# Optimization experiments

Measured on AMD Instinct MI355X. Metric: run time of the kernel, lower is better.

Reference implementation:

```python
import jax, jax.numpy as jnp
import numpy as np

B, N, F, H, HEADS = 2, 256, 64, 64, 4
C = HEADS * H  # n_coefficients (coefficients_mlp is Identity => must equal n_heads*hidden)
EPS = 1e-5
INF = 1e5


def _lin(key, fan_in, fan_out, bias=True):
    k1, k2 = jax.random.split(key)
    w = jax.random.normal(k1, (fan_in, fan_out), jnp.float32) * (1.0 / np.sqrt(fan_in))
    if bias:
        b = jax.random.normal(k2, (fan_out,), jnp.float32) * 0.01
        return w, b
    return w


def setup_inputs() -> dict:
    key = jax.random.key(0)
    ks = jax.random.split(key, 16)
    inp = dict(
        h=jax.random.normal(ks[0], (B, N, F), jnp.float32),
        x=jax.random.normal(ks[1], (B, N, 3), jnp.float32),
        v=jax.random.normal(ks[2], (B, N, 3), jnp.float32),
    )
    inp['edge_w1'], inp['edge_b1'] = _lin(ks[3], 2 * F + 1, H)
    inp['edge_w2'], inp['edge_b2'] = _lin(ks[4], H, H)
    inp['sem_w'], inp['sem_b'] = _lin(ks[5], H, HEADS)
    inp['post_w1'], inp['post_b1'] = _lin(ks[6], C, H)
    inp['post_w2'], inp['post_b2'] = _lin(ks[7], H, H)
    inp['node_w1'], inp['node_b1'] = _lin(ks[8], C + H + F, H)
    inp['node_w2'], inp['node_b2'] = _lin(ks[9], H, F)
    inp['vel_w1'], inp['vel_b1'] = _lin(ks[10], F, H)
    inp['vel_w2'] = _lin(ks[11], H, 1, bias=False) * 0.001  # xavier gain=0.001 analogue
    inp['vmix_w'] = _lin(ks[12], C, 1, bias=False)[:, 0]
    inp['log_gamma'] = -jnp.log(jnp.linspace(1.0, 5.0, HEADS)).astype(jnp.float32)
    return inp


def reference(h, x, v, edge_w1, edge_b1, edge_w2, edge_b2, sem_w, sem_b,
              post_w1, post_b1, post_w2, post_b2, node_w1, node_b1,
              node_w2, node_b2, vel_w1, vel_b1, vel_w2, vmix_w, log_gamma):
    silu = jax.nn.silu
    n = h.shape[-2]
    eye = jnp.eye(n, dtype=h.dtype)[:, :, None]  # [N,N,1] diagonal mask

    # pairwise geometry: entry [i,j] = x_j - x_i
    x_minus_xt = x[..., None, :, :] - x[..., :, None, :]                # [B,N,N,3]
    x_norm = jnp.sqrt((x_minus_xt ** 2).sum(-1, keepdims=True) + EPS)   # [B,N,N,1]

    # pairwise node-feature concat (h_j, h_i) + distance -> edge MLP
    h_j = jnp.broadcast_to(h[..., None, :, :], (B, n, n, F))
    h_i = jnp.broadcast_to(h[..., :, None, :], (B, n, n, F))
    h_cat = jnp.concatenate([h_j, h_i, x_norm], axis=-1)                # [B,N,N,2F+1]
    h_e_mtx = silu(silu(h_cat @ edge_w1 + edge_b1) @ edge_w2 + edge_b2)  # [B,N,N,H]

    # euclidean attention: softmin over j of gamma*dist, diagonal masked out
    dist = (x_norm + INF * eye) * jnp.exp(log_gamma)                    # [B,N,N,heads]
    euclid_att = jax.nn.softmax(-dist, axis=-2)
    # semantic attention: LeakyReLU(0.2) logits, diagonal masked, softmax over j
    sem = jax.nn.leaky_relu(h_e_mtx @ sem_w + sem_b, 0.2) - INF * eye
    sem_att = jax.nn.softmax(sem, axis=-2)
    comb_att = jax.nn.softmax(euclid_att * sem_att, axis=-2)            # [B,N,N,heads]

    # attention-weighted edge features, flattened over (H, heads)
    h_e_att = (h_e_mtx[..., :, None] * comb_att[..., None, :]).reshape(B, n, n, C)

    # spatial attention (coefficients_mlp is Identity)
    unit = x_minus_xt / (x_norm + EPS)                                  # [B,N,N,3]
    # combinations.mean(dim=-3) without materializing [B,N,N,C,3]
    comb_sum = jnp.einsum('bijc,bijd->bicd', h_e_att, unit) / n         # [B,N,C,3]
    comb_norm = (comb_sum ** 2).sum(-1)                                 # [B,N,C]
    h_comb = silu(silu(comb_norm @ post_w1 + post_b1) @ post_w2 + post_b2)

    # delta_v = mean_j (v_mixing over C of combinations)
    delta_v = jnp.einsum('bijc,c,bijd->bid', h_e_att, vmix_w, unit) / n  # [B,N,3]

    h_agg = h_e_att.sum(axis=-2)                                        # sum over j -> [B,N,C]
    out = jnp.concatenate([h, h_agg, h_comb], axis=-1)
    out = silu(silu(out @ node_w1 + node_b1) @ node_w2 + node_b2)
    h_new = h + out                                                     # residual

    # coordinate / velocity update
    v_scale = silu(h_new @ vel_w1 + vel_b1) @ vel_w2                    # [B,N,1]
    v_new = delta_v + v_scale * v
    x_new = x + v_new
    return h_new, x_new, v_new
```

## Files before the change

### kernel.cpp

```cpp
#include <hip/hip_runtime.h>
#include <hip/hip_bf16.h>
#include <math.h>

#define EPSV 1e-5f
#define INFV 1e5f

typedef short bf16x8 __attribute__((ext_vector_type(8)));
typedef float f32x4 __attribute__((ext_vector_type(4)));

__device__ __forceinline__ float rcp_f(float x) { return __builtin_amdgcn_rcpf(x); }
__device__ __forceinline__ float silu_f(float v) { return v * rcp_f(1.0f + __expf(-v)); }

__device__ __forceinline__ unsigned short f2bf(float f) {
  unsigned int u = __float_as_uint(f);
  u = (u + 0x7fffu + ((u >> 16) & 1u)) >> 16;
  return (unsigned short)u;
}
__device__ __forceinline__ float bf2f(unsigned short h) {
  return __uint_as_float(((unsigned int)h) << 16);
}
__device__ __forceinline__ unsigned int pkbf(float a, float b) {
  float2 f2; f2.x = a; f2.y = b;
  __hip_bfloat162 t = __float22bfloat162_rn(f2);
  unsigned int u;
  __builtin_memcpy(&u, &t, 4);
  return u;
}

__device__ __forceinline__ void gemm64(const unsigned short* A_lds, const unsigned short* B_lds,
                                       int w, int l15, int quad, f32x4 acc[4][4]) {
#pragma unroll
  for (int tr = 0; tr < 4; ++tr)
#pragma unroll
    for (int tc = 0; tc < 4; ++tc)
      acc[tr][tc] = (f32x4){0.f, 0.f, 0.f, 0.f};
#pragma unroll
  for (int ms = 0; ms < 64; ms += 32) {
    bf16x8 af[4], bfr[4];
#pragma unroll
    for (int tr = 0; tr < 4; ++tr)
      af[tr] = *reinterpret_cast<const bf16x8*>(&A_lds[(64 * w + 16 * tr + l15) * 72 + ms + quad * 8]);
#pragma unroll
    for (int tc = 0; tc < 4; ++tc)
      bfr[tc] = *reinterpret_cast<const bf16x8*>(&B_lds[(16 * tc + l15) * 72 + ms + quad * 8]);
#pragma unroll
    for (int tr = 0; tr < 4; ++tr)
#pragma unroll
      for (int tc = 0; tc < 4; ++tc)
        acc[tr][tc] = __builtin_amdgcn_mfma_f32_16x16x32_bf16(af[tr], bfr[tc], acc[tr][tc], 0, 0, 0);
  }
}

__global__ __launch_bounds__(512, 2) void k_all(
    const float* __restrict__ h, const float* __restrict__ x, const float* __restrict__ v,
    const float* __restrict__ ew1, const float* __restrict__ eb1,
    const float* __restrict__ ew2, const float* __restrict__ eb2,
    const float* __restrict__ semw, const float* __restrict__ semb,
    const float* __restrict__ pw1, const float* __restrict__ pb1,
    const float* __restrict__ pw2, const float* __restrict__ pb2,
    const float* __restrict__ nw1, const float* __restrict__ nb1,
    const float* __restrict__ nw2, const float* __restrict__ nb2,
    const float* __restrict__ vw1, const float* __restrict__ vb1,
    const float* __restrict__ vw2, const float* __restrict__ vmix,
    const float* __restrict__ lgam, float* __restrict__ out) {

  __shared__ __align__(16) unsigned short TH0[256 * 72];
  __shared__ __align__(16) unsigned short TH1[256 * 72];
  __shared__ __align__(16) char R0[9216];
  __shared__ __align__(16) char R1[9216];
  __shared__ __align__(16) float SD1[2048];
  __shared__ __align__(16) unsigned short E3T[16 * 72];
  __shared__ __align__(16) float4 unit_l[2][256];
  __shared__ float w1dk[64];
  __shared__ float eb1l[64];
  __shared__ __align__(16) float bms[512];

  const int bid = blockIdx.x;
  const int b   = bid >> 7;
  const int ip  = bid & 127;
  const int tid = threadIdx.x;
  const int g   = tid >> 8;
  const int jt  = tid & 255;
  const int i_g = 2 * ip + g;
  const int bi  = (b << 8) | i_g;
  const int bj  = (b << 8) | jt;

  const int w8   = tid >> 6;
  const int lid  = tid & 63;
  const int wg   = w8 & 3;
  const int l15  = lid & 15;
  const int quad = lid >> 4;

  unsigned short* E2Ta = (unsigned short*)R0;
  unsigned short* E2Tb = (unsigned short*)R1;
  unsigned short* THg  = g ? TH1 : TH0;
  char* Rg = g ? R1 : R0;
  float*  sd_g  = g ? SD1 : (float*)R0;
  float4* cat_g = (float4*)Rg;
  float*  cn_g  = (float*)(Rg + 4096);
  float*  hag_g = (float*)(Rg + 5120);
  float4* scS   = (float4*)bms + g * 8;
  float4* scP   = (float4*)bms + 16 + g * 4;
  float4* scD   = (float4*)bms + 24 + g * 4;
  float*  dvs_g = bms + 128 + g * 4;

  const float xi0 = x[bi * 3 + 0], xi1 = x[bi * 3 + 1], xi2 = x[bi * 3 + 2];
  const float dx = x[bj * 3 + 0] - xi0;
  const float dy = x[bj * 3 + 1] - xi1;
  const float dz = x[bj * 3 + 2] - xi2;
  const float dn = sqrtf(dx * dx + dy * dy + dz * dz + EPSV);
  const float invn = rcp_f(dn + EPSV);
  const float ux = dx * invn, uy = dy * invn, uz = dz * invn;
  unit_l[g][jt] = make_float4(ux, uy, uz, dn);

  {
    const float4* hb4 = reinterpret_cast<const float4*>(h + (size_t)(b << 8) * 64);
#pragma unroll
    for (int q = 0; q < 8; ++q) {
      int idx = q * 512 + tid;
      float4 f4 = hb4[idx];
      int row = idx >> 4, c4 = idx & 15;
      uint2 pk;
      pk.x = pkbf(f4.x, f4.y);
      pk.y = pkbf(f4.z, f4.w);
      *reinterpret_cast<uint2*>(&TH0[row * 72 + c4 * 4]) = pk;
    }
  }
#pragma unroll
  for (int q = 0; q < 8; ++q) {
    int idx = q * 512 + tid;
    E2Ta[(idx & 63) * 72 + (idx >> 6)] = f2bf(ew1[idx]);
  }
#pragma unroll
  for (int q = 0; q < 8; ++q) {
    int idx = q * 512 + tid;
    E2Tb[(idx & 63) * 72 + (idx >> 6)] = f2bf(ew2[idx]);
  }
  {
    int n = tid >> 6, kk = tid & 63;
    E3T[n * 72 + kk] = f2bf((n < 4) ? semw[kk * 4 + n] : vmix[kk * 4 + (n - 4)]);
    E3T[(8 + n) * 72 + kk] = 0;
  }
  if (tid < 64) { w1dk[tid] = ew1[128 * 64 + tid]; eb1l[tid] = eb1[tid]; }
  {
    int s = jt >> 6, k = jt & 63;
    const float* hrow = h + (size_t)bi * 64;
    float bp = 0.f;
#pragma unroll
    for (int f2 = 0; f2 < 16; ++f2) {
      int f = s * 16 + f2;
      bp += hrow[f] * ew1[(64 + f) * 64 + k];
    }
    bms[g * 256 + s * 64 + k] = bp;
  }
  __syncthreads();

  f32x4 acc1[2][4];
#pragma unroll
  for (int tr = 0; tr < 2; ++tr)
#pragma unroll
    for (int tc = 0; tc < 4; ++tc)
      acc1[tr][tc] = (f32x4){0.f, 0.f, 0.f, 0.f};
#pragma unroll
  for (int ms = 0; ms < 64; ms += 32) {
    bf16x8 af[2], bfr[4];
#pragma unroll
    for (int tr = 0; tr < 2; ++tr)
      af[tr] = *reinterpret_cast<const bf16x8*>(&TH0[(32 * w8 + 16 * tr + l15) * 72 + ms + quad * 8]);
#pragma unroll
    for (int tc = 0; tc < 4; ++tc)
      bfr[tc] = *reinterpret_cast<const bf16x8*>(&E2Ta[(16 * tc + l15) * 72 + ms + quad * 8]);
#pragma unroll
    for (int tr = 0; tr < 2; ++tr)
#pragma unroll
      for (int tc = 0; tc < 4; ++tc)
        acc1[tr][tc] = __builtin_amdgcn_mfma_f32_16x16x32_bf16(af[tr], bfr[tc], acc1[tr][tc], 0, 0, 0);
  }

#pragma unroll
  for (int tc = 0; tc < 4; ++tc) {
    int kc = 16 * tc + l15;
    float wd = w1dk[kc];
    float eb = eb1l[kc];
    float ak0 = eb + bms[kc] + bms[64 + kc] + bms[128 + kc] + bms[192 + kc];
    float ak1 = eb + bms[256 + kc] + bms[320 + kc] + bms[384 + kc] + bms[448 + kc];
#pragma unroll
    for (int tr = 0; tr < 2; ++tr)
#pragma unroll
      for (int r = 0; r < 4; ++r) {
        int row = 32 * w8 + 16 * tr + quad * 4 + r;
        float a = acc1[tr][tc][r];
        float d0 = unit_l[0][row].w, d1 = unit_l[1][row].w;
        TH0[row * 72 + kc] = f2bf(silu_f(a + ak0 + d0 * wd));
        TH1[row * 72 + kc] = f2bf(silu_f(a + ak1 + d1 * wd));
      }
  }
  __syncthreads();

  f32x4 acc2[4][4];
  gemm64(THg, E2Tb, wg, l15, quad, acc2);
#pragma unroll
  for (int tc = 0; tc < 4; ++tc) {
    float b2 = eb2[16 * tc + l15];
#pragma unroll
    for (int tr = 0; tr < 4; ++tr)
#pragma unroll
      for (int r = 0; r < 4; ++r) {
        int row = 64 * wg + 16 * tr + quad * 4 + r;
        THg[row * 72 + 16 * tc + l15] = f2bf(silu_f(acc2[tr][tc][r] + b2));
      }
  }

  f32x4 acc3[4];
#pragma unroll
  for (int tr = 0; tr < 4; ++tr) acc3[tr] = (f32x4){0.f, 0.f, 0.f, 0.f};
#pragma unroll
  for (int ms = 0; ms < 64; ms += 32) {
    bf16x8 b3 = *reinterpret_cast<const bf16x8*>(&E3T[l15 * 72 + ms + quad * 8]);
#pragma unroll
    for (int tr = 0; tr < 4; ++tr) {
      bf16x8 a3 = *reinterpret_cast<const bf16x8*>(&THg[(64 * wg + 16 * tr + l15) * 72 + ms + quad * 8]);
      acc3[tr] = __builtin_amdgcn_mfma_f32_16x16x32_bf16(a3, b3, acc3[tr], 0, 0, 0);
    }
  }
  if (l15 < 8) {
#pragma unroll
    for (int tr = 0; tr < 4; ++tr)
#pragma unroll
      for (int r = 0; r < 4; ++r)
        sd_g[(64 * wg + 16 * tr + quad * 4 + r) * 8 + l15] = acc3[tr][r];
  }

  float4 s01 = *reinterpret_cast<const float4*>(sd_g + jt * 8);
  float4 s23 = *reinterpret_cast<const float4*>(sd_g + jt * 8 + 4);
  float4 sbv = *reinterpret_cast<const float4*>(semb);
  const float diag = (jt == i_g) ? INFV : 0.0f;
  float4 sl;
  sl.x = s01.x + sbv.x; sl.y = s01.y + sbv.y; sl.z = s01.z + sbv.z; sl.w = s01.w + sbv.w;
  sl.x = ((sl.x > 0.f) ? sl.x : 0.2f * sl.x) - diag;
  sl.y = ((sl.y > 0.f) ? sl.y : 0.2f * sl.y) - diag;
  sl.z = ((sl.z > 0.f) ? sl.z : 0.2f * sl.z) - diag;
  sl.w = ((sl.w > 0.f) ? sl.w : 0.2f * sl.w) - diag;

  float4 lg4 = *reinterpret_cast<const float4*>(lgam);
  const float dni = dn + diag;
  float4 e_eu = make_float4(__expf(-dni * __expf(lg4.x)), __expf(-dni * __expf(lg4.y)),
                            __expf(-dni * __expf(lg4.z)), __expf(-dni * __expf(lg4.w)));
  float4 e_sem = make_float4(__expf(sl.x), __expf(sl.y), __expf(sl.z), __expf(sl.w));

  float4 a8 = e_eu, b8 = e_sem;
#pragma unroll
  for (int off = 32; off >= 1; off >>= 1) {
    a8.x += __shfl_xor(a8.x, off); a8.y += __shfl_xor(a8.y, off);
    a8.z += __shfl_xor(a8.z, off); a8.w += __shfl_xor(a8.w, off);
    b8.x += __shfl_xor(b8.x, off); b8.y += __shfl_xor(b8.y, off);
    b8.z += __shfl_xor(b8.z, off); b8.w += __shfl_xor(b8.w, off);
  }
  if (lid == 0) { scS[wg] = a8; scS[4 + wg] = b8; }
  __syncthreads();
  float4 Se, Ss;
  {
    float4 r0 = scS[0], r1 = scS[1], r2 = scS[2], r3 = scS[3];
    Se = make_float4(r0.x + r1.x + r2.x + r3.x, r0.y + r1.y + r2.y + r3.y,
                     r0.z + r1.z + r2.z + r3.z, r0.w + r1.w + r2.w + r3.w);
    float4 s0 = scS[4], s1 = scS[5], s2 = scS[6], s3 = scS[7];
    Ss = make_float4(s0.x + s1.x + s2.x + s3.x, s0.y + s1.y + s2.y + s3.y,
                     s0.z + s1.z + s2.z + s3.z, s0.w + s1.w + s2.w + s3.w);
  }

  float4 p = make_float4((e_eu.x * rcp_f(Se.x)) * (e_sem.x * rcp_f(Ss.x)),
                         (e_eu.y * rcp_f(Se.y)) * (e_sem.y * rcp_f(Ss.y)),
                         (e_eu.z * rcp_f(Se.z)) * (e_sem.z * rcp_f(Ss.z)),
                         (e_eu.w * rcp_f(Se.w)) * (e_sem.w * rcp_f(Ss.w)));
  float4 ep = make_float4(__expf(p.x), __expf(p.y), __expf(p.z), __expf(p.w));
  float4 sp8 = ep;
#pragma unroll
  for (int off = 32; off >= 1; off >>= 1) {
    sp8.x += __shfl_xor(sp8.x, off); sp8.y += __shfl_xor(sp8.y, off);
    sp8.z += __shfl_xor(sp8.z, off); sp8.w += __shfl_xor(sp8.w, off);
  }
  if (lid == 0) scP[wg] = sp8;
  __syncthreads();
  float4 Sp;
  {
    float4 r0 = scP[0], r1 = scP[1], r2 = scP[2], r3 = scP[3];
    Sp = make_float4(r0.x + r1.x + r2.x + r3.x, r0.y + r1.y + r2.y + r3.y,
                     r0.z + r1.z + r2.z + r3.z, r0.w + r1.w + r2.w + r3.w);
  }
  float4 catt = make_float4(ep.x * rcp_f(Sp.x), ep.y * rcp_f(Sp.y),
                            ep.z * rcp_f(Sp.z), ep.w * rcp_f(Sp.w));
  cat_g[jt] = catt;

  float s = catt.x * s23.x + catt.y * s23.y + catt.z * s23.z + catt.w * s23.w;
  float dvx = s * ux, dvy = s * uy, dvz = s * uz;
#pragma unroll
  for (int off = 32; off >= 1; off >>= 1) {
    dvx += __shfl_xor(dvx, off); dvy += __shfl_xor(dvy, off); dvz += __shfl_xor(dvz, off);
  }
  if (lid == 0) scD[wg] = make_float4(dvx, dvy, dvz, 0.f);
  __syncthreads();
  if (jt == 0) {
    float4 r0 = scD[0], r1 = scD[1], r2 = scD[2], r3 = scD[3];
    const float inv = 1.0f / 256.0f;
    dvs_g[0] = (r0.x + r1.x + r2.x + r3.x) * inv;
    dvs_g[1] = (r0.y + r1.y + r2.y + r3.y) * inv;
    dvs_g[2] = (r0.z + r1.z + r2.z + r3.z) * inv;
  }

  {
    const int jg   = lid >> 2;
    const int ksub = lid & 3;
    const int kb   = 16 * wg + 4 * ksub;
    float agg[4][4], ax[4][4], ay[4][4], az[4][4];
#pragma unroll
    for (int kk = 0; kk < 4; ++kk)
#pragma unroll
      for (int hd = 0; hd < 4; ++hd) {
        agg[kk][hd] = 0.f; ax[kk][hd] = 0.f; ay[kk][hd] = 0.f; az[kk][hd] = 0.f;
      }
#pragma unroll 4
    for (int jr = 0; jr < 16; ++jr) {
      int jj = jr * 16 + jg;
      ushort4 hv4 = *reinterpret_cast<const ushort4*>(&THg[jj * 72 + kb]);
      float4 ca = cat_g[jj];
      float4 u  = unit_l[g][jj];
      float hev[4] = { bf2f(hv4.x), bf2f(hv4.y), bf2f(hv4.z), bf2f(hv4.w) };
#pragma unroll
      for (int kk = 0; kk < 4; ++kk) {
        float c0 = hev[kk] * ca.x, c1 = hev[kk] * ca.y, c2 = hev[kk] * ca.z, c3 = hev[kk] * ca.w;
        agg[kk][0] += c0; agg[kk][1] += c1; agg[kk][2] += c2; agg[kk][3] += c3;
        ax[kk][0] += c0 * u.x; ay[kk][0] += c0 * u.y; az[kk][0] += c0 * u.z;
        ax[kk][1] += c1 * u.x; ay[kk][1] += c1 * u.y; az[kk][1] += c1 * u.z;
        ax[kk][2] += c2 * u.x; ay[kk][2] += c2 * u.y; az[kk][2] += c2 * u.z;
        ax[kk][3] += c3 * u.x; ay[kk][3] += c3 * u.y; az[kk][3] += c3 * u.z;
      }
    }
#pragma unroll
    for (int off = 4; off <= 32; off <<= 1)
#pragma unroll
      for (int kk = 0; kk < 4; ++kk)
#pragma unroll
        for (int hd = 0; hd < 4; ++hd) {
          agg[kk][hd] += __shfl_xor(agg[kk][hd], off);
          ax[kk][hd]  += __shfl_xor(ax[kk][hd], off);
          ay[kk][hd]  += __shfl_xor(ay[kk][hd], off);
          az[kk][hd]  += __shfl_xor(az[kk][hd], off);
        }
    if (jg == 0) {
      const float inv = 1.0f / 256.0f;
#pragma unroll
      for (int kk = 0; kk < 4; ++kk) {
        int k = kb + kk;
        f32x4 cnv, hgv;
#pragma unroll
        for (int hd = 0; hd < 4; ++hd) {
          float cx = ax[kk][hd] * inv, cy = ay[kk][hd] * inv, cz = az[kk][hd] * inv;
          cnv[hd] = cx * cx + cy * cy + cz * cz;
          hgv[hd] = agg[kk][hd];
        }
        *reinterpret_cast<f32x4*>(&cn_g[k * 4])  = cnv;
        *reinterpret_cast<f32x4*>(&hag_g[k * 4]) = hgv;
      }
    }
  }
  __syncthreads();

  {
    const int k = lid;
    float* tmpg = (float*)THg;
    float a1 = 0.f;
#pragma unroll 16
    for (int m2 = 0; m2 < 64; ++m2) {
      int m = 64 * wg + m2;
      a1 += cn_g[m] * pw1[m * 64 + k];
    }
    tmpg[wg * 64 + k] = a1;
    if (wg == 1 || wg == 2) {
      float a2 = 0.f;
      int base = (wg - 1) * 128;
#pragma unroll 16
      for (int m2 = 0; m2 < 128; ++m2) {
        int m = base + m2;
        a2 += hag_g[m] * nw1[(64 + m) * 64 + k];
      }
      tmpg[256 + (wg - 1) * 64 + k] = a2;
    } else if (wg == 3) {
      float a2 = 0.f;
      const float* hrow = h + (size_t)bi * 64;
#pragma unroll 16
      for (int m = 0; m < 64; ++m) a2 += hrow[m] * nw1[m * 64 + k];
      tmpg[384 + k] = a2;
    }
  }
  __syncthreads();

  if (wg == 0) {
    const int k = lid;
    float* tmpg = (float*)THg;
    float* sh2  = tmpg + 512;

    float m1 = silu_f(pb1[k] + tmpg[k] + tmpg[64 + k] + tmpg[128 + k] + tmpg[192 + k]);
    sh2[k] = m1;

    float a = 0.f;
#pragma unroll 16
    for (int m = 0; m < 64; ++m) a += sh2[m] * pw2[m * 64 + k];
    float hcomb = silu_f(pb2[k] + a);
    sh2[64 + k] = hcomb;

    a = nb1[k] + tmpg[256 + k] + tmpg[320 + k] + tmpg[384 + k];
#pragma unroll 16
    for (int m = 0; m < 64; ++m) a += sh2[64 + m] * nw1[(320 + m) * 64 + k];
    sh2[128 + k] = silu_f(a);

    a = 0.f;
#pragma unroll 16
    for (int m = 0; m < 64; ++m) a += sh2[128 + m] * nw2[m * 64 + k];
    float hn = h[(size_t)bi * 64 + k] + silu_f(nb2[k] + a);
    out[(size_t)bi * 64 + k] = hn;
    sh2[192 + k] = hn;

    a = 0.f;
#pragma unroll 16
    for (int m = 0; m < 64; ++m) a += sh2[192 + m] * vw1[m * 64 + k];
    float vh = silu_f(vb1[k] + a) * vw2[k];
#pragma unroll
    for (int off = 32; off >= 1; off >>= 1) vh += __shfl_xor(vh, off);

    if (k == 0) {
      const float xi[3] = {xi0, xi1, xi2};
#pragma unroll
      for (int d = 0; d < 3; ++d) {
        float vn = dvs_g[d] + vh * v[bi * 3 + d];
        out[32768 + bi * 3 + d] = xi[d] + vn;
        out[34304 + bi * 3 + d] = vn;
      }
    }
  }
}

extern "C" void kernel_launch(void* const* d_in, const int* in_sizes, int n_in,
                              void* d_out, int out_size, void* d_ws, size_t ws_size,
                              hipStream_t stream) {
  const float* h    = (const float*)d_in[0];
  const float* x    = (const float*)d_in[1];
  const float* v    = (const float*)d_in[2];
  const float* ew1  = (const float*)d_in[3];
  const float* eb1  = (const float*)d_in[4];
  const float* ew2  = (const float*)d_in[5];
  const float* eb2  = (const float*)d_in[6];
  const float* semw = (const float*)d_in[7];
  const float* semb = (const float*)d_in[8];
  const float* pw1  = (const float*)d_in[9];
  const float* pb1  = (const float*)d_in[10];
  const float* pw2  = (const float*)d_in[11];
  const float* pb2  = (const float*)d_in[12];
  const float* nw1  = (const float*)d_in[13];
  const float* nb1  = (const float*)d_in[14];
  const float* nw2  = (const float*)d_in[15];
  const float* nb2  = (const float*)d_in[16];
  const float* vw1  = (const float*)d_in[17];
  const float* vb1  = (const float*)d_in[18];
  const float* vw2  = (const float*)d_in[19];
  const float* vmix = (const float*)d_in[20];
  const float* lgam = (const float*)d_in[21];
  float* out = (float*)d_out;

  k_all<<<256, 512, 0, stream>>>(h, x, v, ew1, eb1, ew2, eb2, semw, semb,
                                 pw1, pb1, pw2, pb2, nw1, nb1, nw2, nb2,
                                 vw1, vb1, vw2, vmix, lgam, out);
}
```

Measured before the change: 127.1 us.

## Process one node row per block with 256 threads and prefetch tail weights

Each block now handles a single row i with 256 threads, launching 512 blocks instead of 256 blocks of 512 threads that each covered two rows. The first edge-MLP layer goes back to the shared gemm64 helper, and the second LDS activation buffer and the split bias buffer are removed, which shrinks per-block shared memory and should let more blocks sit on each CU. The trade-off is that every block now reloads and converts the full h tile and the edge weight matrices for one row instead of two, doubling that setup work overall. The change also adds early warm-up loads of the node and post MLP weights, kept alive through an asm barrier, to pull them into cache before the serial tail.

```diff
diff --git a/kernel.cpp b/kernel.cpp
--- a/kernel.cpp
+++ b/kernel.cpp
@@ -51,7 +51,7 @@
   }
 }
 
-__global__ __launch_bounds__(512, 2) void k_all(
+__global__ __launch_bounds__(256, 2) void k_all(
     const float* __restrict__ h, const float* __restrict__ x, const float* __restrict__ v,
     const float* __restrict__ ew1, const float* __restrict__ eb1,
     const float* __restrict__ ew2, const float* __restrict__ eb2,
@@ -64,45 +64,49 @@
     const float* __restrict__ vw2, const float* __restrict__ vmix,
     const float* __restrict__ lgam, float* __restrict__ out) {
 
-  __shared__ __align__(16) unsigned short TH0[256 * 72];
-  __shared__ __align__(16) unsigned short TH1[256 * 72];
+  __shared__ __align__(16) unsigned short TH[256 * 72];
   __shared__ __align__(16) char R0[9216];
   __shared__ __align__(16) char R1[9216];
-  __shared__ __align__(16) float SD1[2048];
   __shared__ __align__(16) unsigned short E3T[16 * 72];
-  __shared__ __align__(16) float4 unit_l[2][256];
+  __shared__ __align__(16) float4 unit_l[256];
   __shared__ float w1dk[64];
   __shared__ float eb1l[64];
-  __shared__ __align__(16) float bms[512];
+  __shared__ __align__(16) float bms[256];
 
   const int bid = blockIdx.x;
-  const int b   = bid >> 7;
-  const int ip  = bid & 127;
+  const int b   = bid >> 8;
+  const int i   = bid & 255;
+  const int bi  = bid;
   const int tid = threadIdx.x;
-  const int g   = tid >> 8;
-  const int jt  = tid & 255;
-  const int i_g = 2 * ip + g;
-  const int bi  = (b << 8) | i_g;
-  const int bj  = (b << 8) | jt;
-
-  const int w8   = tid >> 6;
+  const int j   = tid;
+  const int bj  = (b << 8) | j;
+
+  const int w    = tid >> 6;
   const int lid  = tid & 63;
-  const int wg   = w8 & 3;
   const int l15  = lid & 15;
   const int quad = lid >> 4;
 
   unsigned short* E2Ta = (unsigned short*)R0;
   unsigned short* E2Tb = (unsigned short*)R1;
-  unsigned short* THg  = g ? TH1 : TH0;
-  char* Rg = g ? R1 : R0;
-  float*  sd_g  = g ? SD1 : (float*)R0;
-  float4* cat_g = (float4*)Rg;
-  float*  cn_g  = (float*)(Rg + 4096);
-  float*  hag_g = (float*)(Rg + 5120);
-  float4* scS   = (float4*)bms + g * 8;
-  float4* scP   = (float4*)bms + 16 + g * 4;
-  float4* scD   = (float4*)bms + 24 + g * 4;
-  float*  dvs_g = bms + 128 + g * 4;
+  float*  sd    = (float*)R0;
+  float4* cat_l = (float4*)R1;
+  float*  cn_l  = (float*)(R1 + 4096);
+  float*  hag_l = (float*)(R1 + 5120);
+  float4* scS   = (float4*)bms;
+  float4* scP   = (float4*)bms + 8;
+  float4* scD   = (float4*)bms + 12;
+  float*  dvs   = bms + 64;
+
+  float warm = 0.f;
+  {
+#pragma unroll
+    for (int q = 0; q < 4; ++q) warm += pw1[(4 * tid + q) * 16];
+#pragma unroll
+    for (int q = 0; q < 6; ++q) warm += nw1[(6 * tid + q) * 16];
+    warm += pw2[tid * 16] + nw2[tid * 16] + vw1[tid * 16];
+    if (tid < 64) warm += eb2[tid] + pb1[tid] + pb2[tid] + nb1[tid] +
+                          nb2[tid] + vb1[tid] + vw2[tid];
+  }
 
   const float xi0 = x[bi * 3 + 0], xi1 = x[bi * 3 + 1], xi2 = x[bi * 3 + 2];
   const float dx = x[bj * 3 + 0] - xi0;
@@ -111,39 +115,41 @@
   const float dn = sqrtf(dx * dx + dy * dy + dz * dz + EPSV);
   const float invn = rcp_f(dn + EPSV);
   const float ux = dx * invn, uy = dy * invn, uz = dz * invn;
-  unit_l[g][jt] = make_float4(ux, uy, uz, dn);
+  unit_l[j] = make_float4(ux, uy, uz, dn);
 
   {
     const float4* hb4 = reinterpret_cast<const float4*>(h + (size_t)(b << 8) * 64);
 #pragma unroll
-    for (int q = 0; q < 8; ++q) {
-      int idx = q * 512 + tid;
+    for (int q = 0; q < 16; ++q) {
+      int idx = q * 256 + tid;
       float4 f4 = hb4[idx];
       int row = idx >> 4, c4 = idx & 15;
       uint2 pk;
       pk.x = pkbf(f4.x, f4.y);
       pk.y = pkbf(f4.z, f4.w);
-      *reinterpret_cast<uint2*>(&TH0[row * 72 + c4 * 4]) = pk;
-    }
-  }
-#pragma unroll
-  for (int q = 0; q < 8; ++q) {
-    int idx = q * 512 + tid;
+      *reinterpret_cast<uint2*>(&TH[row * 72 + c4 * 4]) = pk;
+    }
+  }
+#pragma unroll
+  for (int q = 0; q < 16; ++q) {
+    int idx = q * 256 + tid;
     E2Ta[(idx & 63) * 72 + (idx >> 6)] = f2bf(ew1[idx]);
   }
 #pragma unroll
-  for (int q = 0; q < 8; ++q) {
-    int idx = q * 512 + tid;
+  for (int q = 0; q < 16; ++q) {
+    int idx = q * 256 + tid;
     E2Tb[(idx & 63) * 72 + (idx >> 6)] = f2bf(ew2[idx]);
   }
-  {
-    int n = tid >> 6, kk = tid & 63;
+#pragma unroll
+  for (int q = 0; q < 2; ++q) {
+    int idx = q * 256 + tid;
+    int n = idx >> 6, kk = idx & 63;
     E3T[n * 72 + kk] = f2bf((n < 4) ? semw[kk * 4 + n] : vmix[kk * 4 + (n - 4)]);
     E3T[(8 + n) * 72 + kk] = 0;
   }
   if (tid < 64) { w1dk[tid] = ew1[128 * 64 + tid]; eb1l[tid] = eb1[tid]; }
   {
-    int s = jt >> 6, k = jt & 63;
+    int s = tid >> 6, k = tid & 63;
     const float* hrow = h + (size_t)bi * 64;
     float bp = 0.f;
 #pragma unroll
@@ -151,54 +157,29 @@
       int f = s * 16 + f2;
       bp += hrow[f] * ew1[(64 + f) * 64 + k];
     }
-    bms[g * 256 + s * 64 + k] = bp;
-  }
-  __syncthreads();
-
-  f32x4 acc1[2][4];
-#pragma unroll
-  for (int tr = 0; tr < 2; ++tr)
-#pragma unroll
-    for (int tc = 0; tc < 4; ++tc)
-      acc1[tr][tc] = (f32x4){0.f, 0.f, 0.f, 0.f};
-#pragma unroll
-  for (int ms = 0; ms < 64; ms += 32) {
-    bf16x8 af[2], bfr[4];
-#pragma unroll
-    for (int tr = 0; tr < 2; ++tr)
-      af[tr] = *reinterpret_cast<const bf16x8*>(&TH0[(32 * w8 + 16 * tr + l15) * 72 + ms + quad * 8]);
-#pragma unroll
-    for (int tc = 0; tc < 4; ++tc)
-      bfr[tc] = *reinterpret_cast<const bf16x8*>(&E2Ta[(16 * tc + l15) * 72 + ms + quad * 8]);
-#pragma unroll
-    for (int tr = 0; tr < 2; ++tr)
-#pragma unroll
-      for (int tc = 0; tc < 4; ++tc)
-        acc1[tr][tc] = __builtin_amdgcn_mfma_f32_16x16x32_bf16(af[tr], bfr[tc], acc1[tr][tc], 0, 0, 0);
-  }
+    bms[s * 64 + k] = bp;
+  }
+  __syncthreads();
+
+  f32x4 acc[4][4];
+  gemm64(TH, E2Ta, w, l15, quad, acc);
 
 #pragma unroll
   for (int tc = 0; tc < 4; ++tc) {
     int kc = 16 * tc + l15;
     float wd = w1dk[kc];
-    float eb = eb1l[kc];
-    float ak0 = eb + bms[kc] + bms[64 + kc] + bms[128 + kc] + bms[192 + kc];
-    float ak1 = eb + bms[256 + kc] + bms[320 + kc] + bms[384 + kc] + bms[448 + kc];
-#pragma unroll
-    for (int tr = 0; tr < 2; ++tr)
+    float ak = eb1l[kc] + bms[kc] + bms[64 + kc] + bms[128 + kc] + bms[192 + kc];
+#pragma unroll
+    for (int tr = 0; tr < 4; ++tr)
 #pragma unroll
       for (int r = 0; r < 4; ++r) {
-        int row = 32 * w8 + 16 * tr + quad * 4 + r;
-        float a = acc1[tr][tc][r];
-        float d0 = unit_l[0][row].w, d1 = unit_l[1][row].w;
-        TH0[row * 72 + kc] = f2bf(silu_f(a + ak0 + d0 * wd));
-        TH1[row * 72 + kc] = f2bf(silu_f(a + ak1 + d1 * wd));
-      }
-  }
-  __syncthreads();
-
-  f32x4 acc2[4][4];
-  gemm64(THg, E2Tb, wg, l15, quad, acc2);
+        int row = 64 * w + 16 * tr + quad * 4 + r;
+        TH[row * 72 + kc] = f2bf(silu_f(acc[tr][tc][r] + ak + unit_l[row].w * wd));
+      }
+  }
+  __syncthreads();
+
+  gemm64(TH, E2Tb, w, l15, quad, acc);
 #pragma unroll
   for (int tc = 0; tc < 4; ++tc) {
     float b2 = eb2[16 * tc + l15];
@@ -206,8 +187,8 @@
     for (int tr = 0; tr < 4; ++tr)
 #pragma unroll
       for (int r = 0; r < 4; ++r) {
-        int row = 64 * wg + 16 * tr + quad * 4 + r;
-        THg[row * 72 + 16 * tc + l15] = f2bf(silu_f(acc2[tr][tc][r] + b2));
+        int row = 64 * w + 16 * tr + quad * 4 + r;
+        TH[row * 72 + 16 * tc + l15] = f2bf(silu_f(acc[tr][tc][r] + b2));
       }
   }
 
@@ -219,7 +200,7 @@
     bf16x8 b3 = *reinterpret_cast<const bf16x8*>(&E3T[l15 * 72 + ms + quad * 8]);
 #pragma unroll
     for (int tr = 0; tr < 4; ++tr) {
-      bf16x8 a3 = *reinterpret_cast<const bf16x8*>(&THg[(64 * wg + 16 * tr + l15) * 72 + ms + quad * 8]);
+      bf16x8 a3 = *reinterpret_cast<const bf16x8*>(&TH[(64 * w + 16 * tr + l15) * 72 + ms + quad * 8]);
       acc3[tr] = __builtin_amdgcn_mfma_f32_16x16x32_bf16(a3, b3, acc3[tr], 0, 0, 0);
     }
   }
@@ -228,13 +209,13 @@
     for (int tr = 0; tr < 4; ++tr)
 #pragma unroll
       for (int r = 0; r < 4; ++r)
-        sd_g[(64 * wg + 16 * tr + quad * 4 + r) * 8 + l15] = acc3[tr][r];
-  }
-
-  float4 s01 = *reinterpret_cast<const float4*>(sd_g + jt * 8);
-  float4 s23 = *reinterpret_cast<const float4*>(sd_g + jt * 8 + 4);
+        sd[(64 * w + 16 * tr + quad * 4 + r) * 8 + l15] = acc3[tr][r];
+  }
+
+  float4 s01 = *reinterpret_cast<const float4*>(sd + j * 8);
+  float4 s23 = *reinterpret_cast<const float4*>(sd + j * 8 + 4);
   float4 sbv = *reinterpret_cast<const float4*>(semb);
-  const float diag = (jt == i_g) ? INFV : 0.0f;
+  const float diag = (j == i) ? INFV : 0.0f;
   float4 sl;
   sl.x = s01.x + sbv.x; sl.y = s01.y + sbv.y; sl.z = s01.z + sbv.z; sl.w = s01.w + sbv.w;
   sl.x = ((sl.x > 0.f) ? sl.x : 0.2f * sl.x) - diag;
@@ -256,7 +237,7 @@
     b8.x += __shfl_xor(b8.x, off); b8.y += __shfl_xor(b8.y, off);
     b8.z += __shfl_xor(b8.z, off); b8.w += __shfl_xor(b8.w, off);
   }
-  if (lid == 0) { scS[wg] = a8; scS[4 + wg] = b8; }
+  if (lid == 0) { scS[w] = a8; scS[4 + w] = b8; }
   __syncthreads();
   float4 Se, Ss;
   {
@@ -279,7 +260,7 @@
     sp8.x += __shfl_xor(sp8.x, off); sp8.y += __shfl_xor(sp8.y, off);
     sp8.z += __shfl_xor(sp8.z, off); sp8.w += __shfl_xor(sp8.w, off);
   }
-  if (lid == 0) scP[wg] = sp8;
+  if (lid == 0) scP[w] = sp8;
   __syncthreads();
   float4 Sp;
   {
@@ -289,7 +270,7 @@
   }
   float4 catt = make_float4(ep.x * rcp_f(Sp.x), ep.y * rcp_f(Sp.y),
                             ep.z * rcp_f(Sp.z), ep.w * rcp_f(Sp.w));
-  cat_g[jt] = catt;
+  cat_l[j] = catt;
 
   float s = catt.x * s23.x + catt.y * s23.y + catt.z * s23.z + catt.w * s23.w;
   float dvx = s * ux, dvy = s * uy, dvz = s * uz;
@@ -297,20 +278,20 @@
   for (int off = 32; off >= 1; off >>= 1) {
     dvx += __shfl_xor(dvx, off); dvy += __shfl_xor(dvy, off); dvz += __shfl_xor(dvz, off);
   }
-  if (lid == 0) scD[wg] = make_float4(dvx, dvy, dvz, 0.f);
-  __syncthreads();
-  if (jt == 0) {
+  if (lid == 0) scD[w] = make_float4(dvx, dvy, dvz, 0.f);
+  __syncthreads();
+  if (j == 0) {
     float4 r0 = scD[0], r1 = scD[1], r2 = scD[2], r3 = scD[3];
     const float inv = 1.0f / 256.0f;
-    dvs_g[0] = (r0.x + r1.x + r2.x + r3.x) * inv;
-    dvs_g[1] = (r0.y + r1.y + r2.y + r3.y) * inv;
-    dvs_g[2] = (r0.z + r1.z + r2.z + r3.z) * inv;
+    dvs[0] = (r0.x + r1.x + r2.x + r3.x) * inv;
+    dvs[1] = (r0.y + r1.y + r2.y + r3.y) * inv;
+    dvs[2] = (r0.z + r1.z + r2.z + r3.z) * inv;
   }
 
   {
     const int jg   = lid >> 2;
     const int ksub = lid & 3;
-    const int kb   = 16 * wg + 4 * ksub;
+    const int kb   = 16 * w + 4 * ksub;
     float agg[4][4], ax[4][4], ay[4][4], az[4][4];
 #pragma unroll
     for (int kk = 0; kk < 4; ++kk)
@@ -321,9 +302,9 @@
 #pragma unroll 4
     for (int jr = 0; jr < 16; ++jr) {
       int jj = jr * 16 + jg;
-      ushort4 hv4 = *reinterpret_cast<const ushort4*>(&THg[jj * 72 + kb]);
-      float4 ca = cat_g[jj];
-      float4 u  = unit_l[g][jj];
+      ushort4 hv4 = *reinterpret_cast<const ushort4*>(&TH[jj * 72 + kb]);
+      float4 ca = cat_l[jj];
+      float4 u  = unit_l[jj];
       float hev[4] = { bf2f(hv4.x), bf2f(hv4.y), bf2f(hv4.z), bf2f(hv4.w) };
 #pragma unroll
       for (int kk = 0; kk < 4; ++kk) {
@@ -358,33 +339,35 @@
           cnv[hd] = cx * cx + cy * cy + cz * cz;
           hgv[hd] = agg[kk][hd];
         }
-        *reinterpret_cast<f32x4*>(&cn_g[k * 4])  = cnv;
-        *reinterpret_cast<f32x4*>(&hag_g[k * 4]) = hgv;
-      }
-    }
-  }
-  __syncthreads();
+        *reinterpret_cast<f32x4*>(&cn_l[k * 4])  = cnv;
+        *reinterpret_cast<f32x4*>(&hag_l[k * 4]) = hgv;
+      }
+    }
+  }
+  __syncthreads();
+
+  asm volatile("" :: "v"(warm));
 
   {
     const int k = lid;
-    float* tmpg = (float*)THg;
+    float* tmpg = (float*)TH;
     float a1 = 0.f;
 #pragma unroll 16
     for (int m2 = 0; m2 < 64; ++m2) {
-      int m = 64 * wg + m2;
-      a1 += cn_g[m] * pw1[m * 64 + k];
-    }
-    tmpg[wg * 64 + k] = a1;
-    if (wg == 1 || wg == 2) {
+      int m = 64 * w + m2;
+      a1 += cn_l[m] * pw1[m * 64 + k];
+    }
+    tmpg[w * 64 + k] = a1;
+    if (w == 1 || w == 2) {
       float a2 = 0.f;
-      int base = (wg - 1) * 128;
+      int base = (w - 1) * 128;
 #pragma unroll 16
       for (int m2 = 0; m2 < 128; ++m2) {
         int m = base + m2;
-        a2 += hag_g[m] * nw1[(64 + m) * 64 + k];
-      }
-      tmpg[256 + (wg - 1) * 64 + k] = a2;
-    } else if (wg == 3) {
+        a2 += hag_l[m] * nw1[(64 + m) * 64 + k];
+      }
+      tmpg[256 + (w - 1) * 64 + k] = a2;
+    } else if (w == 3) {
       float a2 = 0.f;
       const float* hrow = h + (size_t)bi * 64;
 #pragma unroll 16
@@ -394,9 +377,9 @@
   }
   __syncthreads();
 
-  if (wg == 0) {
+  if (w == 0) {
     const int k = lid;
-    float* tmpg = (float*)THg;
+    float* tmpg = (float*)TH;
     float* sh2  = tmpg + 512;
 
     float m1 = silu_f(pb1[k] + tmpg[k] + tmpg[64 + k] + tmpg[128 + k] + tmpg[192 + k]);
@@ -431,7 +414,7 @@
       const float xi[3] = {xi0, xi1, xi2};
 #pragma unroll
       for (int d = 0; d < 3; ++d) {
-        float vn = dvs_g[d] + vh * v[bi * 3 + d];
+        float vn = dvs[d] + vh * v[bi * 3 + d];
         out[32768 + bi * 3 + d] = xi[d] + vn;
         out[34304 + bi * 3 + d] = vn;
       }
@@ -466,7 +449,7 @@
   const float* lgam = (const float*)d_in[21];
   float* out = (float*)d_out;
 
-  k_all<<<256, 512, 0, stream>>>(h, x, v, ew1, eb1, ew2, eb2, semw, semb,
+  k_all<<<512, 256, 0, stream>>>(h, x, v, ew1, eb1, ew2, eb2, semw, semb,
                                  pw1, pb1, pw2, pb2, nw1, nb1, nw2, nb2,
                                  vw1, vb1, vw2, vmix, lgam, out);
 }
```

After: 128.6 us. Within noise of the previous version (+1.2%).
